# Performance work log

Hardware: AMD Instinct MI355X
Metric: run time of the kernel (lower is better)

Reference implementation:

```python
import jax, jax.numpy as jnp
import numpy as np

N = 10000
E = 160000
H = 4
NEG_SLOPE = 0.2


def _edge_softmax(e, dst):
    # e: [E, H] logits; softmax over edges sharing the same dst node
    m = jax.ops.segment_max(e, dst, num_segments=N)          # [N, H]
    m = jnp.where(jnp.isfinite(m), m, 0.0)
    ex = jnp.exp(e - m[dst])                                  # [E, H]
    den = jax.ops.segment_sum(ex, dst, num_segments=N)       # [N, H]
    return ex / (den[dst] + 1e-9)


def _gat_layer(x, src, dst, W, al, ar, resW, edge=None, We=None, ae=None):
    # x: [N, Fin]; W: [Fin, H, D]; al/ar/ae: [H, D]; resW: [Fin, D]
    feat = jnp.einsum('ni,ihd->nhd', x, W)                    # [N, H, D]
    el = jnp.einsum('nhd,hd->nh', feat, al)                   # [N, H]
    er = jnp.einsum('nhd,hd->nh', feat, ar)                   # [N, H]
    e = el[src] + er[dst]                                     # [E, H]
    if edge is not None:
        ef = jnp.einsum('ei,ihd->ehd', edge, We)              # [E, H, D]
        e = e + jnp.einsum('ehd,hd->eh', ef, ae)
    e = jax.nn.leaky_relu(e, NEG_SLOPE)
    alpha = _edge_softmax(e, dst)                             # [E, H]
    msg = feat[src] * alpha[:, :, None]                       # [E, H, D]
    out = jax.ops.segment_sum(msg, dst, num_segments=N)      # [N, H, D]
    return out.mean(axis=1) + x @ resW                        # [N, D]


def setup_inputs() -> dict:
    key = jax.random.key(0)
    ks = jax.random.split(key, 24)
    node_in, edge_in, hid, out = 128, 64, 128, 256
    s = 0.1
    d = {
        'node_feats': jax.random.normal(ks[0], (N, node_in), jnp.float32),
        'edge_feats': jax.random.normal(ks[1], (E, edge_in), jnp.float32),
        'src': jax.random.randint(ks[2], (E,), 0, N, jnp.int32),
        'dst': jax.random.randint(ks[3], (E,), 0, N, jnp.int32),
        # conv1 (with edge feats): node_in -> hid
        'W1':  s * jax.random.normal(ks[4],  (node_in, H, hid), jnp.float32),
        'We1': s * jax.random.normal(ks[5],  (edge_in, H, hid), jnp.float32),
        'al1': s * jax.random.normal(ks[6],  (H, hid), jnp.float32),
        'ar1': s * jax.random.normal(ks[7],  (H, hid), jnp.float32),
        'ae1': s * jax.random.normal(ks[8],  (H, hid), jnp.float32),
        'res1': s * jax.random.normal(ks[9], (node_in, hid), jnp.float32),
        # conv2: hid -> hid
        'W2':  s * jax.random.normal(ks[10], (hid, H, hid), jnp.float32),
        'al2': s * jax.random.normal(ks[11], (H, hid), jnp.float32),
        'ar2': s * jax.random.normal(ks[12], (H, hid), jnp.float32),
        'res2': s * jax.random.normal(ks[13], (hid, hid), jnp.float32),
        # conv3: hid -> hid
        'W3':  s * jax.random.normal(ks[14], (hid, H, hid), jnp.float32),
        'al3': s * jax.random.normal(ks[15], (H, hid), jnp.float32),
        'ar3': s * jax.random.normal(ks[16], (H, hid), jnp.float32),
        'res3': s * jax.random.normal(ks[17], (hid, hid), jnp.float32),
        # conv4: hid -> out
        'W4':  s * jax.random.normal(ks[18], (hid, H, out), jnp.float32),
        'al4': s * jax.random.normal(ks[19], (H, out), jnp.float32),
        'ar4': s * jax.random.normal(ks[20], (H, out), jnp.float32),
        'res4': s * jax.random.normal(ks[21], (hid, out), jnp.float32),
    }
    return d


def reference(node_feats, edge_feats, src, dst,
              W1, We1, al1, ar1, ae1, res1,
              W2, al2, ar2, res2,
              W3, al3, ar3, res3,
              W4, al4, ar4, res4):
    h = jax.nn.relu(_gat_layer(node_feats, src, dst, W1, al1, ar1, res1,
                               edge=edge_feats, We=We1, ae=ae1))
    h = jax.nn.relu(_gat_layer(h, src, dst, W2, al2, ar2, res2))
    h = jax.nn.relu(_gat_layer(h, src, dst, W3, al3, ar3, res3))
    h = jax.nn.relu(_gat_layer(h, src, dst, W4, al4, ar4, res4))
    return h
```

## Files before the change

kernel.cpp:

```cpp
#include <hip/hip_runtime.h>

#define NN 10000
#define EE 160000

#define HB 625
#define GYR 157
#define GB128 (11 * GYR)
#define GB256 (21 * GYR)

typedef __attribute__((ext_vector_type(8))) short bf16x8;
typedef __attribute__((ext_vector_type(4))) float f32x4;
typedef __attribute__((ext_vector_type(2))) float f32x2;
typedef __attribute__((ext_vector_type(8))) float f32x8;
typedef __attribute__((ext_vector_type(16))) float f32x16;

__device__ __forceinline__ short f2b(float f) {
    union { float f; unsigned u; } v; v.f = f;
    unsigned r = v.u + 0x7FFF + ((v.u >> 16) & 1);
    return (short)(r >> 16);
}
__device__ __forceinline__ unsigned char f2q(float f) {
    return (unsigned char)(__builtin_amdgcn_cvt_pk_fp8_f32(f, f, 0, false) & 0xFF);
}

struct PrepParams {
    const float* tsrc[8];
    short* tdst[8];
    int tN[8];
    int tshift[8];
    int tcum4[9];
    const float* W[4]; const float* al[4]; const float* ar[4];
    short* Wc[4]; int Dl[4]; int base[4];
    const float* We1; const float* ae1; float* vbuf;
    const float* node_feats; short* xb;
    const int* dst; int* counts;
    int bWA, bV, bC, bZ, nblk;
};
__global__ __launch_bounds__(256) void prep_kernel(PrepParams P) {
    int blk = blockIdx.x, tid = threadIdx.x;
    if (blk < P.bWA) {
        int t = blk * 256 + tid;
        if (t >= P.tcum4[8]) return;
        int i = 0;
        #pragma unroll
        for (int j = 1; j < 8; ++j) i += (t >= P.tcum4[j]);
        int local = t - P.tcum4[i];
        int N = P.tN[i], sh = P.tshift[i];
        int k = local >> (sh - 2);
        int nq = local & ((N >> 2) - 1);
        float4 v = *(const float4*)(P.tsrc[i] + (size_t)k * N + nq * 4);
        short* d = P.tdst[i] + (size_t)nq * 4 * 128 + k;
        d[0] = f2b(v.x); d[128] = f2b(v.y); d[256] = f2b(v.z); d[384] = f2b(v.w);
    } else if (blk < P.bV) {
        int bl = blk - P.bWA;
        int l = bl >> 7, within = bl & 127;
        int wv = tid >> 6, ln = tid & 63;
        int wid = within * 4 + wv;
        int k = wid >> 2, h = wid & 3;
        int D = P.Dl[l];
        const float* w = P.W[l] + ((size_t)k * 4 + h) * D;
        const float* a = P.al[l] + (size_t)h * D;
        const float* r = P.ar[l] + (size_t)h * D;
        float sa, sr;
        if (D == 128) {
            float2 w2 = ((const float2*)w)[ln];
            float2 a2 = ((const float2*)a)[ln];
            float2 r2 = ((const float2*)r)[ln];
            sa = w2.x * a2.x + w2.y * a2.y;
            sr = w2.x * r2.x + w2.y * r2.y;
        } else {
            float4 w4 = ((const float4*)w)[ln];
            float4 a4 = ((const float4*)a)[ln];
            float4 r4 = ((const float4*)r)[ln];
            sa = w4.x * a4.x + w4.y * a4.y + w4.z * a4.z + w4.w * a4.w;
            sr = w4.x * r4.x + w4.y * r4.y + w4.z * r4.z + w4.w * r4.w;
        }
        #pragma unroll
        for (int o = 32; o; o >>= 1) { sa += __shfl_xor(sa, o); sr += __shfl_xor(sr, o); }
        if (ln == 0) {
            P.Wc[l][(size_t)(P.base[l] + h) * 128 + k]     = f2b(sa);
            P.Wc[l][(size_t)(P.base[l] + 4 + h) * 128 + k] = f2b(sr);
        }
    } else if (blk < P.bC) {
        int bl = blk - P.bV;
        int wv = tid >> 6, ln = tid & 63;
        int i = bl * 4 + wv;
        #pragma unroll
        for (int h = 0; h < 4; ++h) {
            const float* w = P.We1 + ((size_t)i * 4 + h) * 128;
            const float* a = P.ae1 + (size_t)h * 128;
            float2 w2 = ((const float2*)w)[ln];
            float2 a2 = ((const float2*)a)[ln];
            float s = w2.x * a2.x + w2.y * a2.y;
            #pragma unroll
            for (int o = 32; o; o >>= 1) s += __shfl_xor(s, o);
            if (ln == 0) P.vbuf[i * 4 + h] = s;
        }
    } else if (blk < P.bZ) {
        int t = (blk - P.bC) * 256 + tid;
        if (t < NN * 32) {
            float4 v = ((const float4*)P.node_feats)[t];
            uint2 pk;
            pk.x = (unsigned short)f2b(v.x) | ((unsigned)(unsigned short)f2b(v.y) << 16);
            pk.y = (unsigned short)f2b(v.z) | ((unsigned)(unsigned short)f2b(v.w) << 16);
            ((uint2*)P.xb)[t] = pk;
        }
    } else {
        int e = (blk - P.bZ) * 256 + tid;
        if (e < EE) atomicAdd(&P.counts[P.dst[e]], 1);
    }
}

template <int D>
__device__ __forceinline__ void gemm_body(const short* __restrict__ A,
                                          const short* __restrict__ Bt,
                                          unsigned char* __restrict__ featq,
                                          float* __restrict__ y,
                                          float* __restrict__ elr,
                                          int M, int bx, int by) {
    constexpr int HD = 4 * D;
    int wave = threadIdx.x >> 6, lane = threadIdx.x & 63;
    int m0 = by * 64;
    int n0 = bx * 64 + wave * 16;
    int r = lane & 15, quad = lane >> 4;
    f32x4 acc[4] = {};
    const short* bp = Bt + (size_t)(n0 + r) * 128 + quad * 8;
    #pragma unroll
    for (int k0 = 0; k0 < 128; k0 += 32) {
        bf16x8 bfrag = *(const bf16x8*)(bp + k0);
        #pragma unroll
        for (int mt = 0; mt < 4; ++mt) {
            int gm = m0 + mt * 16 + r;
            bf16x8 afrag = {};
            if (gm < M) afrag = *(const bf16x8*)(A + (size_t)gm * 128 + k0 + quad * 8);
            acc[mt] = __builtin_amdgcn_mfma_f32_16x16x32_bf16(afrag, bfrag, acc[mt], 0, 0, 0);
        }
    }
    int col = n0 + r;
    #pragma unroll
    for (int mt = 0; mt < 4; ++mt) {
        #pragma unroll
        for (int rr = 0; rr < 4; ++rr) {
            int gm = m0 + mt * 16 + quad * 4 + rr;
            if (gm >= M) continue;
            float v = acc[mt][rr];
            if (col < HD)              featq[(size_t)gm * HD + col] = f2q(v);
            else if (col < HD + D)     y[(size_t)gm * D + (col - HD)] = v;
            else if (col < HD + D + 8) elr[(size_t)gm * 8 + (col - HD - D)] = v;
        }
    }
}

template <int D>
__global__ __launch_bounds__(256) void gemm_fused(const short* __restrict__ A,
                                                  const short* __restrict__ Bt,
                                                  unsigned char* __restrict__ featq,
                                                  float* __restrict__ y,
                                                  float* __restrict__ elr,
                                                  int M) {
    gemm_body<D>(A, Bt, featq, y, elr, M, blockIdx.x, blockIdx.y);
}

__device__ __forceinline__ void scan_body(const int* __restrict__ counts,
                                          int* __restrict__ off,
                                          int* __restrict__ cur) {
    __shared__ int part[256];
    const int n = NN;
    int tid = threadIdx.x;
    int lo = tid * 40;
    int4 r[10];
    int s = 0;
    #pragma unroll
    for (int q = 0; q < 10; ++q) {
        int idx = lo + q * 4;
        int4 v = make_int4(0, 0, 0, 0);
        if (idx + 3 < n) v = *(const int4*)(counts + idx);
        r[q] = v;
        s += v.x + v.y + v.z + v.w;
    }
    part[tid] = s;
    __syncthreads();
    for (int o = 1; o < 256; o <<= 1) {
        int v = (tid >= o) ? part[tid - o] : 0;
        __syncthreads();
        part[tid] += v;
        __syncthreads();
    }
    int run = tid ? part[tid - 1] : 0;
    #pragma unroll
    for (int q = 0; q < 10; ++q) {
        int4 v = r[q], o4;
        o4.x = run; run += v.x;
        o4.y = run; run += v.y;
        o4.z = run; run += v.z;
        o4.w = run; run += v.w;
        int idx = lo + q * 4;
        if (idx + 3 < n) { *(int4*)(off + idx) = o4; *(int4*)(cur + idx) = o4; }
    }
    if (tid == 255) off[n] = part[255];
}

__global__ __launch_bounds__(256) void gemm1_extra_scan(const float* __restrict__ ef,
                                                        const float* __restrict__ vbuf,
                                                        float* __restrict__ extraU,
                                                        const short* __restrict__ A,
                                                        const short* __restrict__ Bt,
                                                        unsigned char* __restrict__ featq,
                                                        float* __restrict__ y,
                                                        float* __restrict__ elr,
                                                        const int* __restrict__ counts,
                                                        int* __restrict__ off,
                                                        int* __restrict__ cur) {
    int vb = blockIdx.x;
    if (vb < HB) {
        __shared__ float vs[256];
        vs[threadIdx.x] = vbuf[threadIdx.x];
        __syncthreads();
        int e = vb * 256 + threadIdx.x;
        if (e < EE) {
            float a0 = 0.f, a1 = 0.f, a2 = 0.f, a3 = 0.f;
            const float4* e4 = (const float4*)(ef + (size_t)e * 64);
            #pragma unroll
            for (int c = 0; c < 16; ++c) {
                float4 x = e4[c];
                int b = c * 16;
                a0 += x.x * vs[b + 0] + x.y * vs[b + 4] + x.z * vs[b + 8] + x.w * vs[b + 12];
                a1 += x.x * vs[b + 1] + x.y * vs[b + 5] + x.z * vs[b + 9] + x.w * vs[b + 13];
                a2 += x.x * vs[b + 2] + x.y * vs[b + 6] + x.z * vs[b + 10] + x.w * vs[b + 14];
                a3 += x.x * vs[b + 3] + x.y * vs[b + 7] + x.z * vs[b + 11] + x.w * vs[b + 15];
            }
            float4 o; o.x = a0; o.y = a1; o.z = a2; o.w = a3;
            *(float4*)(extraU + (size_t)e * 4) = o;
        }
    } else if (vb < HB + GB128) {
        int b = vb - HB;
        gemm_body<128>(A, Bt, featq, y, elr, NN, b % 11, b / 11);
    } else {
        scan_body(counts, off, cur);
    }
}

__global__ __launch_bounds__(256) void fill_extra(const int* __restrict__ src,
                                                  const int* __restrict__ dst,
                                                  int* __restrict__ cur,
                                                  const float* __restrict__ extraU,
                                                  int* __restrict__ ssrc,
                                                  float* __restrict__ extra, int E) {
    int e = blockIdx.x * 256 + threadIdx.x;
    if (e >= E) return;
    int p = atomicAdd(&cur[dst[e]], 1);
    ssrc[p] = src[e];
    *(float4*)(extra + (size_t)p * 4) = *(const float4*)(extraU + (size_t)e * 4);
}

__device__ __forceinline__ f32x8 accum8q(f32x8 a, uint2 v, float w) {
    f32x2 p;
    p = __builtin_amdgcn_cvt_pk_f32_fp8(v.x, false); a[0] += w * p.x; a[1] += w * p.y;
    p = __builtin_amdgcn_cvt_pk_f32_fp8(v.x, true);  a[2] += w * p.x; a[3] += w * p.y;
    p = __builtin_amdgcn_cvt_pk_f32_fp8(v.y, false); a[4] += w * p.x; a[5] += w * p.y;
    p = __builtin_amdgcn_cvt_pk_f32_fp8(v.y, true);  a[6] += w * p.x; a[7] += w * p.y;
    return a;
}
__device__ __forceinline__ f32x16 accum16q(f32x16 a, uint4 v, float w) {
    f32x2 p;
    p = __builtin_amdgcn_cvt_pk_f32_fp8(v.x, false); a[0] += w * p.x; a[1] += w * p.y;
    p = __builtin_amdgcn_cvt_pk_f32_fp8(v.x, true);  a[2] += w * p.x; a[3] += w * p.y;
    p = __builtin_amdgcn_cvt_pk_f32_fp8(v.y, false); a[4] += w * p.x; a[5] += w * p.y;
    p = __builtin_amdgcn_cvt_pk_f32_fp8(v.y, true);  a[6] += w * p.x; a[7] += w * p.y;
    p = __builtin_amdgcn_cvt_pk_f32_fp8(v.z, false); a[8] += w * p.x; a[9] += w * p.y;
    p = __builtin_amdgcn_cvt_pk_f32_fp8(v.z, true);  a[10] += w * p.x; a[11] += w * p.y;
    p = __builtin_amdgcn_cvt_pk_f32_fp8(v.w, false); a[12] += w * p.x; a[13] += w * p.y;
    p = __builtin_amdgcn_cvt_pk_f32_fp8(v.w, true);  a[14] += w * p.x; a[15] += w * p.y;
    return a;
}

struct SM64 { float ev0, ev1, ev2, ev3; int sx0, sx1, sx2, sx3; float sc; };

template <bool HAS_EXTRA>
__device__ __forceinline__ SM64 softmax64(int r0, int deg, int h, int jh, float erh,
                                          const float* __restrict__ elr,
                                          const float* __restrict__ extra,
                                          const int* __restrict__ ssrc) {
    SM64 R;
    float a0 = -1e30f, a1 = -1e30f, a2 = -1e30f, a3 = -1e30f;
    int sx0 = 0, sx1 = 0, sx2 = 0, sx3 = 0;
    auto lg = [&](int j, int& sx, float& a) {
        if (j < deg) {
            int idx = r0 + j;
            sx = ssrc[idx];
            float v = elr[(size_t)sx * 8 + h] + erh;
            if (HAS_EXTRA) v += extra[(size_t)idx * 4 + h];
            a = v > 0.f ? v : 0.2f * v;
        }
    };
    lg(jh, sx0, a0);
    if (deg > 16) lg(jh + 16, sx1, a1);
    if (deg > 32) lg(jh + 32, sx2, a2);
    if (deg > 48) lg(jh + 48, sx3, a3);
    float m = fmaxf(fmaxf(a0, a1), fmaxf(a2, a3));
    #pragma unroll
    for (int o = 1; o < 16; o <<= 1) m = fmaxf(m, __shfl_xor(m, o));
    R.ev0 = __expf(a0 - m); R.ev1 = __expf(a1 - m);
    R.ev2 = __expf(a2 - m); R.ev3 = __expf(a3 - m);
    float ss = R.ev0 + R.ev1 + R.ev2 + R.ev3;
    #pragma unroll
    for (int o = 1; o < 16; o <<= 1) ss += __shfl_xor(ss, o);
    R.sc = 0.25f / (ss + 1e-9f);
    R.sx0 = sx0; R.sx1 = sx1; R.sx2 = sx2; R.sx3 = sx3;
    return R;
}

template <bool HAS_EXTRA>
__global__ __launch_bounds__(256) void gat128(const unsigned char* __restrict__ featq,
                                              const float* __restrict__ elr,
                                              const float* __restrict__ extra,
                                              const int* __restrict__ ssrc,
                                              const int* __restrict__ off,
                                              const float* __restrict__ yres,
                                              short* __restrict__ ybf) {
    int wv = threadIdx.x >> 6, ln = threadIdx.x & 63;
    int n = blockIdx.x * 4 + wv;
    int r0 = off[n], deg = off[n + 1] - r0;
    int h = ln >> 4, jh = ln & 15;
    float erh = elr[(size_t)n * 8 + 4 + h];
    f32x8 acc = {};
    const unsigned char* basep = featq + ln * 8;
    float sc;

    if (deg <= 64) {
        SM64 R = softmax64<HAS_EXTRA>(r0, deg, h, jh, erh, elr, extra, ssrc);
        sc = R.sc;
        int hh = h << 4;
        auto blk16 = [&](float ee, int si, int cnt) {
            int c = 0;
            for (; c + 4 <= cnt; c += 4) {
                float w0 = __shfl(ee, hh | c),       w1 = __shfl(ee, hh | (c + 1));
                float w2 = __shfl(ee, hh | (c + 2)), w3 = __shfl(ee, hh | (c + 3));
                int s0 = __shfl(si, c),     s1 = __shfl(si, c + 1);
                int s2 = __shfl(si, c + 2), s3 = __shfl(si, c + 3);
                uint2 v0 = *(const uint2*)(basep + (size_t)s0 * 512);
                uint2 v1 = *(const uint2*)(basep + (size_t)s1 * 512);
                uint2 v2 = *(const uint2*)(basep + (size_t)s2 * 512);
                uint2 v3 = *(const uint2*)(basep + (size_t)s3 * 512);
                acc = accum8q(acc, v0, w0); acc = accum8q(acc, v1, w1);
                acc = accum8q(acc, v2, w2); acc = accum8q(acc, v3, w3);
            }
            for (; c < cnt; ++c) {
                float w = __shfl(ee, hh | c);
                int s = __shfl(si, c);
                uint2 v = *(const uint2*)(basep + (size_t)s * 512);
                acc = accum8q(acc, v, w);
            }
        };
        blk16(R.ev0, R.sx0, deg < 16 ? deg : 16);
        if (deg > 16) blk16(R.ev1, R.sx1, deg < 32 ? deg - 16 : 16);
        if (deg > 32) blk16(R.ev2, R.sx2, deg < 48 ? deg - 32 : 16);
        if (deg > 48) blk16(R.ev3, R.sx3, deg - 48);
    } else {
        auto lgt = [&](int c) {
            int s = ssrc[r0 + c];
            float v = elr[(size_t)s * 8 + h] + erh;
            if (HAS_EXTRA) v += extra[(size_t)(r0 + c) * 4 + h];
            return v > 0.f ? v : 0.2f * v;
        };
        float m = -1e30f;
        for (int c = 0; c < deg; ++c) m = fmaxf(m, lgt(c));
        float ss = 0.f;
        for (int c = 0; c < deg; ++c) ss += __expf(lgt(c) - m);
        sc = 0.25f / (ss + 1e-9f);
        for (int c = 0; c < deg; ++c) {
            float w = __expf(lgt(c) - m);
            int s = ssrc[r0 + c];
            uint2 v = *(const uint2*)(basep + (size_t)s * 512);
            acc = accum8q(acc, v, w);
        }
    }

    f32x8 t;
    #pragma unroll
    for (int i = 0; i < 8; ++i) {
        float v = acc[i] * sc;
        v += __shfl_xor(v, 16);
        v += __shfl_xor(v, 32);
        t[i] = v;
    }
    if (ln < 16) {
        const float* yr = yres + (size_t)n * 128 + ln * 8;
        float4 y0 = *(const float4*)yr;
        float4 y1 = *(const float4*)(yr + 4);
        float o0 = fmaxf(y0.x + t[0], 0.f), o1 = fmaxf(y0.y + t[1], 0.f);
        float o2 = fmaxf(y0.z + t[2], 0.f), o3 = fmaxf(y0.w + t[3], 0.f);
        float o4 = fmaxf(y1.x + t[4], 0.f), o5 = fmaxf(y1.y + t[5], 0.f);
        float o6 = fmaxf(y1.z + t[6], 0.f), o7 = fmaxf(y1.w + t[7], 0.f);
        uint4 pa;
        pa.x = (unsigned short)f2b(o0) | ((unsigned)(unsigned short)f2b(o1) << 16);
        pa.y = (unsigned short)f2b(o2) | ((unsigned)(unsigned short)f2b(o3) << 16);
        pa.z = (unsigned short)f2b(o4) | ((unsigned)(unsigned short)f2b(o5) << 16);
        pa.w = (unsigned short)f2b(o6) | ((unsigned)(unsigned short)f2b(o7) << 16);
        *(uint4*)(ybf + (size_t)n * 128 + ln * 8) = pa;
    }
}

__global__ __launch_bounds__(256) void gat256(const unsigned char* __restrict__ featq,
                                              const float* __restrict__ elr,
                                              const int* __restrict__ ssrc,
                                              const int* __restrict__ off,
                                              const float* __restrict__ yres,
                                              float* __restrict__ yout) {
    __shared__ float red[2][16 * 17];
    int wv = threadIdx.x >> 6, ln = threadIdx.x & 63;
    int slot = wv >> 1, half = wv & 1;
    int n = blockIdx.x * 2 + slot;
    int r0 = off[n], deg = off[n + 1] - r0;
    int h = ln >> 4, jh = ln & 15;
    float erh = elr[(size_t)n * 8 + 4 + h];
    f32x16 acc = {};
    const unsigned char* basep = featq + ln * 16;
    float sc;

    if (deg <= 64) {
        SM64 R = softmax64<false>(r0, deg, h, jh, erh, elr, nullptr, ssrc);
        sc = R.sc;
        int hh = h << 4;
        auto blk16 = [&](float ee, int si, int cnt) {
            int c = half;
            for (; c + 6 < cnt; c += 8) {
                float w0 = __shfl(ee, hh | c),       w1 = __shfl(ee, hh | (c + 2));
                float w2 = __shfl(ee, hh | (c + 4)), w3 = __shfl(ee, hh | (c + 6));
                int s0 = __shfl(si, c),     s1 = __shfl(si, c + 2);
                int s2 = __shfl(si, c + 4), s3 = __shfl(si, c + 6);
                uint4 v0 = *(const uint4*)(basep + (size_t)s0 * 1024);
                uint4 v1 = *(const uint4*)(basep + (size_t)s1 * 1024);
                uint4 v2 = *(const uint4*)(basep + (size_t)s2 * 1024);
                uint4 v3 = *(const uint4*)(basep + (size_t)s3 * 1024);
                acc = accum16q(acc, v0, w0); acc = accum16q(acc, v1, w1);
                acc = accum16q(acc, v2, w2); acc = accum16q(acc, v3, w3);
            }
            for (; c < cnt; c += 2) {
                float w = __shfl(ee, hh | c);
                int s = __shfl(si, c);
                uint4 v = *(const uint4*)(basep + (size_t)s * 1024);
                acc = accum16q(acc, v, w);
            }
        };
        blk16(R.ev0, R.sx0, deg < 16 ? deg : 16);
        if (deg > 16) blk16(R.ev1, R.sx1, (deg < 32 ? deg : 32) - 16);
        if (deg > 32) blk16(R.ev2, R.sx2, (deg < 48 ? deg : 48) - 32);
        if (deg > 48) blk16(R.ev3, R.sx3, deg - 48);
    } else {
        auto lgt = [&](int c) {
            int s = ssrc[r0 + c];
            float v = elr[(size_t)s * 8 + h] + erh;
            return v > 0.f ? v : 0.2f * v;
        };
        float m = -1e30f;
        for (int c = 0; c < deg; ++c) m = fmaxf(m, lgt(c));
        float ss = 0.f;
        for (int c = 0; c < deg; ++c) ss += __expf(lgt(c) - m);
        sc = 0.25f / (ss + 1e-9f);
        for (int c = half; c < deg; c += 2) {
            float w = __expf(lgt(c) - m);
            int s = ssrc[r0 + c];
            uint4 v = *(const uint4*)(basep + (size_t)s * 1024);
            acc = accum16q(acc, v, w);
        }
    }

    f32x16 t;
    #pragma unroll
    for (int i = 0; i < 16; ++i) {
        float v = acc[i] * sc;
        v += __shfl_xor(v, 16);
        v += __shfl_xor(v, 32);
        t[i] = v;
    }
    if (half == 1 && ln < 16) {
        #pragma unroll
        for (int i = 0; i < 16; ++i) red[slot][ln * 17 + i] = t[i];
    }
    __syncthreads();
    if (half == 0 && ln < 16) {
        const float* yr = yres + (size_t)n * 256 + ln * 16;
        float* yo = yout + (size_t)n * 256 + ln * 16;
        #pragma unroll
        for (int q = 0; q < 4; ++q) {
            float4 ya = *(const float4*)(yr + 4 * q);
            float4 ov;
            ov.x = fmaxf(ya.x + t[4 * q + 0] + red[slot][ln * 17 + 4 * q + 0], 0.f);
            ov.y = fmaxf(ya.y + t[4 * q + 1] + red[slot][ln * 17 + 4 * q + 1], 0.f);
            ov.z = fmaxf(ya.z + t[4 * q + 2] + red[slot][ln * 17 + 4 * q + 2], 0.f);
            ov.w = fmaxf(ya.w + t[4 * q + 3] + red[slot][ln * 17 + 4 * q + 3], 0.f);
            *(float4*)(yo + 4 * q) = ov;
        }
    }
}

extern "C" void kernel_launch(void* const* d_in, const int* in_sizes, int n_in,
                              void* d_out, int out_size, void* d_ws, size_t ws_size,
                              hipStream_t stream) {
    const float* node_feats = (const float*)d_in[0];
    const float* edge_feats = (const float*)d_in[1];
    const int*   src        = (const int*)d_in[2];
    const int*   dst        = (const int*)d_in[3];
    const float* W1   = (const float*)d_in[4];
    const float* We1  = (const float*)d_in[5];
    const float* al1  = (const float*)d_in[6];
    const float* ar1  = (const float*)d_in[7];
    const float* ae1  = (const float*)d_in[8];
    const float* res1 = (const float*)d_in[9];
    const float* W2   = (const float*)d_in[10];
    const float* al2  = (const float*)d_in[11];
    const float* ar2  = (const float*)d_in[12];
    const float* res2 = (const float*)d_in[13];
    const float* W3   = (const float*)d_in[14];
    const float* al3  = (const float*)d_in[15];
    const float* ar3  = (const float*)d_in[16];
    const float* res3 = (const float*)d_in[17];
    const float* W4   = (const float*)d_in[18];
    const float* al4  = (const float*)d_in[19];
    const float* ar4  = (const float*)d_in[20];
    const float* res4 = (const float*)d_in[21];

    char* ws = (char*)d_ws;
    auto alloc = [&](size_t bytes) -> char* {
        char* p = ws;
        ws += (bytes + 255) & ~(size_t)255;
        return p;
    };
    int*   counts  = (int*)alloc((size_t)NN * 4);
    int*   offsets = (int*)alloc((size_t)(NN + 1) * 4);
    int*   cursor  = (int*)alloc((size_t)(NN + 1) * 4);
    int*   ssrc    = (int*)alloc((size_t)EE * 4);
    unsigned char* featq = (unsigned char*)alloc((size_t)NN * 1024);
    float* xA      = (float*)alloc((size_t)NN * 128 * 4);
    short* xb      = (short*)alloc((size_t)NN * 128 * 2);
    float* elr     = (float*)alloc((size_t)NN * 8 * 4);
    float* extra   = (float*)alloc((size_t)EE * 4 * 4);
    float* extraU  = (float*)alloc((size_t)EE * 4 * 4);
    float* vbuf    = (float*)alloc(1024);
    short* Wc1     = (short*)alloc((size_t)704 * 128 * 2);
    short* Wc2     = (short*)alloc((size_t)704 * 128 * 2);
    short* Wc3     = (short*)alloc((size_t)704 * 128 * 2);
    short* Wc4     = (short*)alloc((size_t)1344 * 128 * 2);

    PrepParams P;
    P.tsrc[0] = W1;   P.tdst[0] = Wc1;              P.tN[0] = 512;  P.tshift[0] = 9;
    P.tsrc[1] = W2;   P.tdst[1] = Wc2;              P.tN[1] = 512;  P.tshift[1] = 9;
    P.tsrc[2] = W3;   P.tdst[2] = Wc3;              P.tN[2] = 512;  P.tshift[2] = 9;
    P.tsrc[3] = W4;   P.tdst[3] = Wc4;              P.tN[3] = 1024; P.tshift[3] = 10;
    P.tsrc[4] = res1; P.tdst[4] = Wc1 + 512 * 128;  P.tN[4] = 128;  P.tshift[4] = 7;
    P.tsrc[5] = res2; P.tdst[5] = Wc2 + 512 * 128;  P.tN[5] = 128;  P.tshift[5] = 7;
    P.tsrc[6] = res3; P.tdst[6] = Wc3 + 512 * 128;  P.tN[6] = 128;  P.tshift[6] = 7;
    P.tsrc[7] = res4; P.tdst[7] = Wc4 + 1024 * 128; P.tN[7] = 256;  P.tshift[7] = 8;
    P.tcum4[0] = 0;
    for (int i = 0; i < 8; ++i) P.tcum4[i + 1] = P.tcum4[i] + P.tN[i] * 128 / 4;
    P.W[0] = W1; P.W[1] = W2; P.W[2] = W3; P.W[3] = W4;
    P.al[0] = al1; P.al[1] = al2; P.al[2] = al3; P.al[3] = al4;
    P.ar[0] = ar1; P.ar[1] = ar2; P.ar[2] = ar3; P.ar[3] = ar4;
    P.Wc[0] = Wc1; P.Wc[1] = Wc2; P.Wc[2] = Wc3; P.Wc[3] = Wc4;
    P.Dl[0] = 128; P.Dl[1] = 128; P.Dl[2] = 128; P.Dl[3] = 256;
    P.base[0] = 640; P.base[1] = 640; P.base[2] = 640; P.base[3] = 1280;
    P.We1 = We1; P.ae1 = ae1; P.vbuf = vbuf;
    P.node_feats = node_feats; P.xb = xb;
    P.dst = dst; P.counts = counts;
    P.bWA = (P.tcum4[8] + 255) / 256;
    P.bV  = P.bWA + 512;
    P.bC  = P.bV + 16;
    P.bZ  = P.bC + (NN * 32 + 255) / 256;
    P.nblk = P.bZ + HB;

    float* out = (float*)d_out;

    hipMemsetAsync(counts, 0, (size_t)NN * 4, stream);
    prep_kernel<<<P.nblk, 256, 0, stream>>>(P);
    gemm1_extra_scan<<<HB + GB128 + 1, 256, 0, stream>>>(
        edge_feats, vbuf, extraU, xb, Wc1, featq, xA, elr, counts, offsets, cursor);
    fill_extra<<<HB, 256, 0, stream>>>(src, dst, cursor, extraU, ssrc, extra, EE);

    dim3 g128(11, GYR);
    dim3 g256(21, GYR);
    gat128<true><<<NN / 4, 256, 0, stream>>>(featq, elr, extra, ssrc, offsets, xA, xb);
    gemm_fused<128><<<g128, 256, 0, stream>>>(xb, Wc2, featq, xA, elr, NN);
    gat128<false><<<NN / 4, 256, 0, stream>>>(featq, elr, nullptr, ssrc, offsets, xA, xb);
    gemm_fused<128><<<g128, 256, 0, stream>>>(xb, Wc3, featq, xA, elr, NN);
    gat128<false><<<NN / 4, 256, 0, stream>>>(featq, elr, nullptr, ssrc, offsets, xA, xb);
    gemm_fused<256><<<g256, 256, 0, stream>>>(xb, Wc4, featq, out, elr, NN);
    gat256<<<NN / 2, 256, 0, stream>>>(featq, elr, ssrc, offsets, out, out);
}
```

Baseline: 335.8 us.

## Vectorize GEMM epilogue stores and widen gat128 gathers to 16-byte loads

The GEMM swaps its MFMA operands so each lane holds four consecutive output columns of one row. It can then emit packed 4-byte fp8 stores and float4 stores instead of scattered single-element writes. In gat128, each lane now gathers 16 fp8 features (uint4) and the two half-waves process alternating edges. The halves are combined with an extra cross-lane reduction. This aims to cut gather instruction count and store transactions, at the cost of more shuffle reductions and masked tail iterations.

```diff
diff --git a/kernel.cpp b/kernel.cpp
--- a/kernel.cpp
+++ b/kernel.cpp
@@ -18,9 +18,6 @@
     union { float f; unsigned u; } v; v.f = f;
     unsigned r = v.u + 0x7FFF + ((v.u >> 16) & 1);
     return (short)(r >> 16);
-}
-__device__ __forceinline__ unsigned char f2q(float f) {
-    return (unsigned char)(__builtin_amdgcn_cvt_pk_fp8_f32(f, f, 0, false) & 0xFF);
 }
 
 struct PrepParams {
@@ -133,20 +130,25 @@
             int gm = m0 + mt * 16 + r;
             bf16x8 afrag = {};
             if (gm < M) afrag = *(const bf16x8*)(A + (size_t)gm * 128 + k0 + quad * 8);
-            acc[mt] = __builtin_amdgcn_mfma_f32_16x16x32_bf16(afrag, bfrag, acc[mt], 0, 0, 0);
-        }
-    }
-    int col = n0 + r;
+            acc[mt] = __builtin_amdgcn_mfma_f32_16x16x32_bf16(bfrag, afrag, acc[mt], 0, 0, 0);
+        }
+    }
+    int c4 = n0 + quad * 4;
     #pragma unroll
     for (int mt = 0; mt < 4; ++mt) {
-        #pragma unroll
-        for (int rr = 0; rr < 4; ++rr) {
-            int gm = m0 + mt * 16 + quad * 4 + rr;
-            if (gm >= M) continue;
-            float v = acc[mt][rr];
-            if (col < HD)              featq[(size_t)gm * HD + col] = f2q(v);
-            else if (col < HD + D)     y[(size_t)gm * D + (col - HD)] = v;
-            else if (col < HD + D + 8) elr[(size_t)gm * 8 + (col - HD - D)] = v;
+        int gm = m0 + mt * 16 + r;
+        if (gm >= M) continue;
+        float v0 = acc[mt][0], v1 = acc[mt][1], v2 = acc[mt][2], v3 = acc[mt][3];
+        if (c4 < HD) {
+            unsigned p = __builtin_amdgcn_cvt_pk_fp8_f32(v0, v1, 0, false);
+            p = __builtin_amdgcn_cvt_pk_fp8_f32(v2, v3, p, true);
+            *(unsigned*)(featq + (size_t)gm * HD + c4) = p;
+        } else if (c4 < HD + D) {
+            float4 o; o.x = v0; o.y = v1; o.z = v2; o.w = v3;
+            *(float4*)(y + (size_t)gm * D + (c4 - HD)) = o;
+        } else if (c4 < HD + D + 8) {
+            float4 o; o.x = v0; o.y = v1; o.z = v2; o.w = v3;
+            *(float4*)(elr + (size_t)gm * 8 + (c4 - HD - D)) = o;
         }
     }
 }
@@ -253,14 +255,6 @@
     *(float4*)(extra + (size_t)p * 4) = *(const float4*)(extraU + (size_t)e * 4);
 }
 
-__device__ __forceinline__ f32x8 accum8q(f32x8 a, uint2 v, float w) {
-    f32x2 p;
-    p = __builtin_amdgcn_cvt_pk_f32_fp8(v.x, false); a[0] += w * p.x; a[1] += w * p.y;
-    p = __builtin_amdgcn_cvt_pk_f32_fp8(v.x, true);  a[2] += w * p.x; a[3] += w * p.y;
-    p = __builtin_amdgcn_cvt_pk_f32_fp8(v.y, false); a[4] += w * p.x; a[5] += w * p.y;
-    p = __builtin_amdgcn_cvt_pk_f32_fp8(v.y, true);  a[6] += w * p.x; a[7] += w * p.y;
-    return a;
-}
 __device__ __forceinline__ f32x16 accum16q(f32x16 a, uint4 v, float w) {
     f32x2 p;
     p = __builtin_amdgcn_cvt_pk_f32_fp8(v.x, false); a[0] += w * p.x; a[1] += w * p.y;
@@ -322,34 +316,36 @@
     int n = blockIdx.x * 4 + wv;
     int r0 = off[n], deg = off[n + 1] - r0;
     int h = ln >> 4, jh = ln & 15;
+    int g = ln >> 5, l5 = ln & 31;
+    int hw = (l5 >> 3) << 4;
     float erh = elr[(size_t)n * 8 + 4 + h];
-    f32x8 acc = {};
-    const unsigned char* basep = featq + ln * 8;
-    float sc;
+    f32x16 acc = {};
+    const unsigned char* basep = featq + l5 * 16;
+    float scl;
 
     if (deg <= 64) {
         SM64 R = softmax64<HAS_EXTRA>(r0, deg, h, jh, erh, elr, extra, ssrc);
-        sc = R.sc;
-        int hh = h << 4;
+        scl = __shfl(R.sc, hw);
         auto blk16 = [&](float ee, int si, int cnt) {
             int c = 0;
             for (; c + 4 <= cnt; c += 4) {
-                float w0 = __shfl(ee, hh | c),       w1 = __shfl(ee, hh | (c + 1));
-                float w2 = __shfl(ee, hh | (c + 2)), w3 = __shfl(ee, hh | (c + 3));
-                int s0 = __shfl(si, c),     s1 = __shfl(si, c + 1);
-                int s2 = __shfl(si, c + 2), s3 = __shfl(si, c + 3);
-                uint2 v0 = *(const uint2*)(basep + (size_t)s0 * 512);
-                uint2 v1 = *(const uint2*)(basep + (size_t)s1 * 512);
-                uint2 v2 = *(const uint2*)(basep + (size_t)s2 * 512);
-                uint2 v3 = *(const uint2*)(basep + (size_t)s3 * 512);
-                acc = accum8q(acc, v0, w0); acc = accum8q(acc, v1, w1);
-                acc = accum8q(acc, v2, w2); acc = accum8q(acc, v3, w3);
+                float w0 = __shfl(ee, hw | (c + g));
+                float w1 = __shfl(ee, hw | (c + 2 + g));
+                int s0 = __shfl(si, c + g);
+                int s1 = __shfl(si, c + 2 + g);
+                uint4 v0 = *(const uint4*)(basep + (size_t)s0 * 512);
+                uint4 v1 = *(const uint4*)(basep + (size_t)s1 * 512);
+                acc = accum16q(acc, v0, w0);
+                acc = accum16q(acc, v1, w1);
             }
-            for (; c < cnt; ++c) {
-                float w = __shfl(ee, hh | c);
-                int s = __shfl(si, c);
-                uint2 v = *(const uint2*)(basep + (size_t)s * 512);
-                acc = accum8q(acc, v, w);
+            for (; c < cnt; c += 2) {
+                int j = c + g;
+                float msk = j < cnt ? 1.f : 0.f;
+                int jc = j < cnt ? j : c;
+                float w = __shfl(ee, hw | jc) * msk;
+                int s = __shfl(si, jc);
+                uint4 v = *(const uint4*)(basep + (size_t)s * 512);
+                acc = accum16q(acc, v, w);
             }
         };
         blk16(R.ev0, R.sx0, deg < 16 ? deg : 16);
@@ -357,47 +353,52 @@
         if (deg > 32) blk16(R.ev2, R.sx2, deg < 48 ? deg - 32 : 16);
         if (deg > 48) blk16(R.ev3, R.sx3, deg - 48);
     } else {
+        int hg = l5 >> 3;
+        float erg = elr[(size_t)n * 8 + 4 + hg];
         auto lgt = [&](int c) {
             int s = ssrc[r0 + c];
-            float v = elr[(size_t)s * 8 + h] + erh;
-            if (HAS_EXTRA) v += extra[(size_t)(r0 + c) * 4 + h];
+            float v = elr[(size_t)s * 8 + hg] + erg;
+            if (HAS_EXTRA) v += extra[(size_t)(r0 + c) * 4 + hg];
             return v > 0.f ? v : 0.2f * v;
         };
         float m = -1e30f;
         for (int c = 0; c < deg; ++c) m = fmaxf(m, lgt(c));
         float ss = 0.f;
         for (int c = 0; c < deg; ++c) ss += __expf(lgt(c) - m);
-        sc = 0.25f / (ss + 1e-9f);
-        for (int c = 0; c < deg; ++c) {
+        scl = 0.25f / (ss + 1e-9f);
+        for (int c = g; c < deg; c += 2) {
             float w = __expf(lgt(c) - m);
             int s = ssrc[r0 + c];
-            uint2 v = *(const uint2*)(basep + (size_t)s * 512);
-            acc = accum8q(acc, v, w);
-        }
-    }
-
-    f32x8 t;
-    #pragma unroll
-    for (int i = 0; i < 8; ++i) {
-        float v = acc[i] * sc;
+            uint4 v = *(const uint4*)(basep + (size_t)s * 512);
+            acc = accum16q(acc, v, w);
+        }
+    }
+
+    f32x16 t;
+    #pragma unroll
+    for (int i = 0; i < 16; ++i) {
+        float v = acc[i] * scl;
+        v += __shfl_xor(v, 8);
         v += __shfl_xor(v, 16);
         v += __shfl_xor(v, 32);
         t[i] = v;
     }
-    if (ln < 16) {
-        const float* yr = yres + (size_t)n * 128 + ln * 8;
-        float4 y0 = *(const float4*)yr;
-        float4 y1 = *(const float4*)(yr + 4);
-        float o0 = fmaxf(y0.x + t[0], 0.f), o1 = fmaxf(y0.y + t[1], 0.f);
-        float o2 = fmaxf(y0.z + t[2], 0.f), o3 = fmaxf(y0.w + t[3], 0.f);
-        float o4 = fmaxf(y1.x + t[4], 0.f), o5 = fmaxf(y1.y + t[5], 0.f);
-        float o6 = fmaxf(y1.z + t[6], 0.f), o7 = fmaxf(y1.w + t[7], 0.f);
-        uint4 pa;
-        pa.x = (unsigned short)f2b(o0) | ((unsigned)(unsigned short)f2b(o1) << 16);
-        pa.y = (unsigned short)f2b(o2) | ((unsigned)(unsigned short)f2b(o3) << 16);
-        pa.z = (unsigned short)f2b(o4) | ((unsigned)(unsigned short)f2b(o5) << 16);
-        pa.w = (unsigned short)f2b(o6) | ((unsigned)(unsigned short)f2b(o7) << 16);
-        *(uint4*)(ybf + (size_t)n * 128 + ln * 8) = pa;
+    if (ln < 8) {
+        int d0 = ln * 16;
+        const float* yr = yres + (size_t)n * 128 + d0;
+        unsigned pk[8];
+        #pragma unroll
+        for (int q = 0; q < 8; ++q) {
+            float ya = yr[2 * q], yb = yr[2 * q + 1];
+            float o0 = fmaxf(ya + t[2 * q], 0.f);
+            float o1 = fmaxf(yb + t[2 * q + 1], 0.f);
+            pk[q] = (unsigned short)f2b(o0) | ((unsigned)(unsigned short)f2b(o1) << 16);
+        }
+        uint4 pa, pb;
+        pa.x = pk[0]; pa.y = pk[1]; pa.z = pk[2]; pa.w = pk[3];
+        pb.x = pk[4]; pb.y = pk[5]; pb.z = pk[6]; pb.w = pk[7];
+        *(uint4*)(ybf + (size_t)n * 128 + d0) = pa;
+        *(uint4*)(ybf + (size_t)n * 128 + d0 + 8) = pb;
     }
 }
 
```

Result: slower. 344.6 us (+2.6%).

## Schedule GAT node aggregation in descending-degree order via degree-bucket permutation

Applied to the files above, without the earlier changes.

The scan block now builds a histogram of in-degrees (clamped at 63) and writes a node permutation sorted by descending degree. The GAT aggregation kernels read this permutation to pick their node, so heavy nodes are launched first and waves within a block have similar degrees. This targets load imbalance and tail effects in the edge-gather kernels. The cost is extra shared-memory atomics in the single scan block, an indirection load per wave, and less locality between consecutive nodes when writing outputs.

```diff
diff --git a/kernel.cpp b/kernel.cpp
--- a/kernel.cpp
+++ b/kernel.cpp
@@ -163,10 +163,14 @@
 
 __device__ __forceinline__ void scan_body(const int* __restrict__ counts,
                                           int* __restrict__ off,
-                                          int* __restrict__ cur) {
+                                          int* __restrict__ cur,
+                                          int* __restrict__ nodeperm) {
     __shared__ int part[256];
+    __shared__ int hist[64], hbase[64], hcnt[64];
     const int n = NN;
     int tid = threadIdx.x;
+    if (tid < 64) { hist[tid] = 0; hcnt[tid] = 0; }
+    __syncthreads();
     int lo = tid * 40;
     int4 r[10];
     int s = 0;
@@ -177,6 +181,10 @@
         if (idx + 3 < n) v = *(const int4*)(counts + idx);
         r[q] = v;
         s += v.x + v.y + v.z + v.w;
+        atomicAdd(&hist[v.x < 63 ? v.x : 63], 1);
+        atomicAdd(&hist[v.y < 63 ? v.y : 63], 1);
+        atomicAdd(&hist[v.z < 63 ? v.z : 63], 1);
+        atomicAdd(&hist[v.w < 63 ? v.w : 63], 1);
     }
     part[tid] = s;
     __syncthreads();
@@ -198,6 +206,25 @@
         if (idx + 3 < n) { *(int4*)(off + idx) = o4; *(int4*)(cur + idx) = o4; }
     }
     if (tid == 255) off[n] = part[255];
+    if (tid < 64) {
+        int acc = 0;
+        for (int b2 = tid + 1; b2 < 64; ++b2) acc += hist[b2];
+        hbase[tid] = acc;
+    }
+    __syncthreads();
+    #pragma unroll
+    for (int q = 0; q < 10; ++q) {
+        int4 v = r[q];
+        int idx = lo + q * 4;
+        int b0 = v.x < 63 ? v.x : 63;
+        int b1 = v.y < 63 ? v.y : 63;
+        int b2 = v.z < 63 ? v.z : 63;
+        int b3 = v.w < 63 ? v.w : 63;
+        nodeperm[hbase[b0] + atomicAdd(&hcnt[b0], 1)] = idx;
+        nodeperm[hbase[b1] + atomicAdd(&hcnt[b1], 1)] = idx + 1;
+        nodeperm[hbase[b2] + atomicAdd(&hcnt[b2], 1)] = idx + 2;
+        nodeperm[hbase[b3] + atomicAdd(&hcnt[b3], 1)] = idx + 3;
+    }
 }
 
 __global__ __launch_bounds__(256) void gemm1_extra_scan(const float* __restrict__ ef,
@@ -210,7 +237,8 @@
                                                         float* __restrict__ elr,
                                                         const int* __restrict__ counts,
                                                         int* __restrict__ off,
-                                                        int* __restrict__ cur) {
+                                                        int* __restrict__ cur,
+                                                        int* __restrict__ nodeperm) {
     int vb = blockIdx.x;
     if (vb < HB) {
         __shared__ float vs[256];
@@ -236,7 +264,7 @@
         int b = vb - HB;
         gemm_body<128>(A, Bt, featq, y, elr, NN, b % 11, b / 11);
     } else {
-        scan_body(counts, off, cur);
+        scan_body(counts, off, cur, nodeperm);
     }
 }
 
@@ -316,10 +344,11 @@
                                               const float* __restrict__ extra,
                                               const int* __restrict__ ssrc,
                                               const int* __restrict__ off,
+                                              const int* __restrict__ nodeperm,
                                               const float* __restrict__ yres,
                                               short* __restrict__ ybf) {
     int wv = threadIdx.x >> 6, ln = threadIdx.x & 63;
-    int n = blockIdx.x * 4 + wv;
+    int n = nodeperm[blockIdx.x * 4 + wv];
     int r0 = off[n], deg = off[n + 1] - r0;
     int h = ln >> 4, jh = ln & 15;
     float erh = elr[(size_t)n * 8 + 4 + h];
@@ -405,12 +434,13 @@
                                               const float* __restrict__ elr,
                                               const int* __restrict__ ssrc,
                                               const int* __restrict__ off,
+                                              const int* __restrict__ nodeperm,
                                               const float* __restrict__ yres,
                                               float* __restrict__ yout) {
     __shared__ float red[2][16 * 17];
     int wv = threadIdx.x >> 6, ln = threadIdx.x & 63;
     int slot = wv >> 1, half = wv & 1;
-    int n = blockIdx.x * 2 + slot;
+    int n = nodeperm[blockIdx.x * 2 + slot];
     int r0 = off[n], deg = off[n + 1] - r0;
     int h = ln >> 4, jh = ln & 15;
     float erh = elr[(size_t)n * 8 + 4 + h];
@@ -530,6 +560,7 @@
     int*   counts  = (int*)alloc((size_t)NN * 4);
     int*   offsets = (int*)alloc((size_t)(NN + 1) * 4);
     int*   cursor  = (int*)alloc((size_t)(NN + 1) * 4);
+    int*   nodeperm = (int*)alloc((size_t)NN * 4);
     int*   ssrc    = (int*)alloc((size_t)EE * 4);
     unsigned char* featq = (unsigned char*)alloc((size_t)NN * 1024);
     float* xA      = (float*)alloc((size_t)NN * 128 * 4);
@@ -574,16 +605,20 @@
     hipMemsetAsync(counts, 0, (size_t)NN * 4, stream);
     prep_kernel<<<P.nblk, 256, 0, stream>>>(P);
     gemm1_extra_scan<<<HB + GB128 + 1, 256, 0, stream>>>(
-        edge_feats, vbuf, extraU, xb, Wc1, featq, xA, elr, counts, offsets, cursor);
+        edge_feats, vbuf, extraU, xb, Wc1, featq, xA, elr, counts, offsets, cursor,
+        nodeperm);
     fill_extra<<<HB, 256, 0, stream>>>(src, dst, cursor, extraU, ssrc, extra, EE);
 
     dim3 g128(11, GYR);
     dim3 g256(21, GYR);
-    gat128<true><<<NN / 4, 256, 0, stream>>>(featq, elr, extra, ssrc, offsets, xA, xb);
+    gat128<true><<<NN / 4, 256, 0, stream>>>(featq, elr, extra, ssrc, offsets,
+                                             nodeperm, xA, xb);
     gemm_fused<128><<<g128, 256, 0, stream>>>(xb, Wc2, featq, xA, elr, NN);
-    gat128<false><<<NN / 4, 256, 0, stream>>>(featq, elr, nullptr, ssrc, offsets, xA, xb);
+    gat128<false><<<NN / 4, 256, 0, stream>>>(featq, elr, nullptr, ssrc, offsets,
+                                              nodeperm, xA, xb);
     gemm_fused<128><<<g128, 256, 0, stream>>>(xb, Wc3, featq, xA, elr, NN);
-    gat128<false><<<NN / 4, 256, 0, stream>>>(featq, elr, nullptr, ssrc, offsets, xA, xb);
+    gat128<false><<<NN / 4, 256, 0, stream>>>(featq, elr, nullptr, ssrc, offsets,
+                                              nodeperm, xA, xb);
     gemm_fused<256><<<g256, 256, 0, stream>>>(xb, Wc4, featq, out, elr, NN);
-    gat256<<<NN / 2, 256, 0, stream>>>(featq, elr, ssrc, offsets, out, out);
-}
+    gat256<<<NN / 2, 256, 0, stream>>>(featq, elr, ssrc, offsets, nodeperm, out, out);
+}
```

New measurement: 335.1 us, median of 2. No clear change (-0.2%).
